# Performance work log

Measured on AMD Instinct MI355X. Metric: run time of the kernel, lower is better.

The kernel has to match this reference:

```python
import jax, jax.numpy as jnp
import numpy as np

M = 128        # max_units (units // 2)
BETA = 15.0

def setup_inputs() -> dict:
    key = jax.random.key(0)
    k1, k2 = jax.random.split(key)
    x = jax.random.normal(k1, (2048, 512), dtype=jnp.float32)
    w = jax.random.normal(k2, (512, 256), dtype=jnp.float32) * 0.05  # 'random_normal' init scale
    return {"x": x, "w": w}

def reference(x, w):
    # s[b, f, u] = beta * (x[b, f] + w[f, u]); shape (B, F, U)
    s = BETA * (x[:, :, None] + w[None, :, :])
    # smooth max over features for first M units
    hv = jax.nn.logsumexp(s[..., :M], axis=1) / BETA          # (B, M)
    # smooth min over features for remaining units
    hw = -jax.nn.logsumexp(-s[..., M:], axis=1) / BETA         # (B, U-M)
    return jnp.concatenate([hv, hw], axis=1)                   # (B, U)
```

## Files before the change

kernel.cpp:

```cpp
#include <hip/hip_runtime.h>

#define B_DIM 2048
#define F_DIM 512
#define U_DIM 256

constexpr float K_L2E = 21.64042561333445f;
constexpr float INV_K = 1.0f / K_L2E;

using short8 = __attribute__((ext_vector_type(8))) short;
using f32x4  = __attribute__((ext_vector_type(4))) float;

__device__ __forceinline__ unsigned short f2bf(float f) {
    unsigned u = __float_as_uint(f);
    return (unsigned short)((u + 0x7FFFu + ((u >> 16) & 1u)) >> 16);
}

__global__ __launch_bounds__(256)
void prep_w(const float* __restrict__ w, unsigned short* __restrict__ ew) {
    const int c   = (blockIdx.x << 8) + threadIdx.x;
    const int cl  = c & 63;
    const int ckb = (c >> 6) & 15;
    const int cut = c >> 10;
    const int u   = (cut << 4) + (cl & 15);
    const int gw  = cl >> 4;
    const int fb  = (ckb << 5) + (gw << 3);
    const float s = (u < 128) ? K_L2E : -K_L2E;
    short8 cc;
#pragma unroll
    for (int i = 0; i < 8; ++i)
        cc[i] = (short)f2bf(exp2f(s * w[(fb + i) * U_DIM + u]));
    reinterpret_cast<short8*>(ew)[c] = cc;
}

__global__ __launch_bounds__(256)
void fused_k(const float* __restrict__ x, const unsigned short* __restrict__ ew,
             float* __restrict__ out) {
    __shared__ short8 sA[1024];
    __shared__ float  sst[16];

    const int tid  = threadIdx.x;
    const int wv   = tid >> 6;
    const int lane = tid & 63;
    const int rt   = blockIdx.x >> 2;
    const int utq  = blockIdx.x & 3;
    const int mode = utq >> 1;
    const int ut   = (utq << 2) + wv;

    const int   kb_w = lane >> 2;
    const int   g_w  = lane & 3;
    const float sgn  = mode ? -1.f : 1.f;

#pragma unroll
    for (int j = 0; j < 4; ++j) {
        const int row = (wv << 2) + j;
        const float4* xr = reinterpret_cast<const float4*>(x + (rt * 16 + row) * F_DIM);
        float4 v0 = xr[lane * 2];
        float4 v1 = xr[lane * 2 + 1];
        float t[8] = {sgn * v0.x, sgn * v0.y, sgn * v0.z, sgn * v0.w,
                      sgn * v1.x, sgn * v1.y, sgn * v1.z, sgn * v1.w};
        float hi = t[0];
#pragma unroll
        for (int i = 1; i < 8; ++i) hi = fmaxf(hi, t[i]);
#pragma unroll
        for (int off = 32; off; off >>= 1) hi = fmaxf(hi, __shfl_xor(hi, off));
        if (lane == 0) sst[row] = hi;
        short8 cb;
#pragma unroll
        for (int i = 0; i < 8; ++i) cb[i] = (short)f2bf(exp2f(K_L2E * (t[i] - hi)));
        sA[(kb_w << 6) + ((row + (g_w << 4)) ^ (kb_w & 7))] = cb;
    }
    __syncthreads();

    const short8* B = reinterpret_cast<const short8*>(ew) + (ut << 4) * 64 + lane;
    f32x4 acc = {0.f, 0.f, 0.f, 0.f};
#pragma unroll
    for (int kb = 0; kb < 16; ++kb) {
        short8 a = sA[(kb << 6) + (lane ^ (kb & 7))];
        acc = __builtin_amdgcn_mfma_f32_16x16x32_bf16(a, B[kb * 64], acc, 0, 0, 0);
    }

    const int j    = lane & 15;
    const int quad = lane >> 4;
#pragma unroll
    for (int r = 0; r < 4; ++r) {
        const int row = (quad << 2) + r;
        float res = sst[row] + __log2f(acc[r]) * INV_K;
        out[(rt * 16 + row) * U_DIM + (ut << 4) + j] = mode ? -res : res;
    }
}

extern "C" void kernel_launch(void* const* d_in, const int* in_sizes, int n_in,
                              void* d_out, int out_size, void* d_ws, size_t ws_size,
                              hipStream_t stream) {
    const float* x = (const float*)d_in[0];
    const float* w = (const float*)d_in[1];
    float* out = (float*)d_out;
    unsigned short* ew = (unsigned short*)d_ws;

    prep_w<<<64, 256, 0, stream>>>(w, ew);
    fused_k<<<512, 256, 0, stream>>>(x, ew, out);
}
```

Before: 14.96 us.

## Fuse weight exponentiation into main kernel, dropping separate prep launch

Removes the prep_w kernel that precomputed bf16 exp(±k·w) into workspace. Each wave now loads its own 16-column slice of w directly, exponentiates it and converts to bf16 in registers before the MFMA loop. This saves one kernel launch and the workspace round trip. In exchange, every block (128 row tiles per column group) redoes the exp work on w, and the strided fp32 loads of w are less coalesced than the pre-packed layout.

Result: slower. 15.56 us (+4.0%).

```diff
diff --git a/kernel.cpp b/kernel.cpp
--- a/kernel.cpp
+++ b/kernel.cpp
@@ -16,25 +16,8 @@
 }
 
 __global__ __launch_bounds__(256)
-void prep_w(const float* __restrict__ w, unsigned short* __restrict__ ew) {
-    const int c   = (blockIdx.x << 8) + threadIdx.x;
-    const int cl  = c & 63;
-    const int ckb = (c >> 6) & 15;
-    const int cut = c >> 10;
-    const int u   = (cut << 4) + (cl & 15);
-    const int gw  = cl >> 4;
-    const int fb  = (ckb << 5) + (gw << 3);
-    const float s = (u < 128) ? K_L2E : -K_L2E;
-    short8 cc;
-#pragma unroll
-    for (int i = 0; i < 8; ++i)
-        cc[i] = (short)f2bf(exp2f(s * w[(fb + i) * U_DIM + u]));
-    reinterpret_cast<short8*>(ew)[c] = cc;
-}
-
-__global__ __launch_bounds__(256)
-void fused_k(const float* __restrict__ x, const unsigned short* __restrict__ ew,
-             float* __restrict__ out) {
+void fused1_k(const float* __restrict__ x, const float* __restrict__ w,
+              float* __restrict__ out) {
     __shared__ short8 sA[1024];
     __shared__ float  sst[16];
 
@@ -69,14 +52,26 @@
         for (int i = 0; i < 8; ++i) cb[i] = (short)f2bf(exp2f(K_L2E * (t[i] - hi)));
         sA[(kb_w << 6) + ((row + (g_w << 4)) ^ (kb_w & 7))] = cb;
     }
+
+    const int   uc = (ut << 4) + (lane & 15);
+    const int   g  = lane >> 4;
+    const float sw = mode ? -K_L2E : K_L2E;
+    short8 bfr[16];
+#pragma unroll
+    for (int kb = 0; kb < 16; ++kb) {
+        const float* wp = w + (32 * kb + 8 * g) * U_DIM + uc;
+#pragma unroll
+        for (int i = 0; i < 8; ++i)
+            bfr[kb][i] = (short)f2bf(exp2f(sw * wp[i * U_DIM]));
+    }
+
     __syncthreads();
 
-    const short8* B = reinterpret_cast<const short8*>(ew) + (ut << 4) * 64 + lane;
     f32x4 acc = {0.f, 0.f, 0.f, 0.f};
 #pragma unroll
     for (int kb = 0; kb < 16; ++kb) {
         short8 a = sA[(kb << 6) + (lane ^ (kb & 7))];
-        acc = __builtin_amdgcn_mfma_f32_16x16x32_bf16(a, B[kb * 64], acc, 0, 0, 0);
+        acc = __builtin_amdgcn_mfma_f32_16x16x32_bf16(a, bfr[kb], acc, 0, 0, 0);
     }
 
     const int j    = lane & 15;
@@ -95,8 +90,5 @@
     const float* x = (const float*)d_in[0];
     const float* w = (const float*)d_in[1];
     float* out = (float*)d_out;
-    unsigned short* ew = (unsigned short*)d_ws;
-
-    prep_w<<<64, 256, 0, stream>>>(w, ew);
-    fused_k<<<512, 256, 0, stream>>>(x, ew, out);
+    fused1_k<<<512, 256, 0, stream>>>(x, w, out);
 }
```
